# Kernel optimization log

Hardware: AMD Instinct MI355X
Metric: run time of the kernel (lower is better)

Reference implementation:

```python
import jax, jax.numpy as jnp
import numpy as np


def setup_inputs() -> dict:
    key = jax.random.key(0)
    k1, k2, k3, k4 = jax.random.split(key, 4)
    N, E, F_IN, HID, C = 50000, 1600000, 256, 64, 16
    x = jax.random.normal(k1, (N, F_IN), dtype=jnp.float32)
    edge_index = jax.random.randint(k2, (2, E), 0, N, dtype=jnp.int64)
    W1 = jax.random.normal(k3, (F_IN, HID), dtype=jnp.float32) * (1.0 / np.sqrt(F_IN))
    b1 = jnp.zeros((HID,), dtype=jnp.float32)
    W2 = jax.random.normal(k4, (HID, C), dtype=jnp.float32) * (1.0 / np.sqrt(HID))
    b2 = jnp.zeros((C,), dtype=jnp.float32)
    return {"x": x, "edge_index": edge_index, "W1": W1, "b1": b1, "W2": W2, "b2": b2}


def reference(x, edge_index, W1, b1, W2, b2):
    N = x.shape[0]
    # Add self-loops (GCNConv default)
    loops = jnp.arange(N, dtype=edge_index.dtype)
    row = jnp.concatenate([edge_index[0], loops])  # targets
    col = jnp.concatenate([edge_index[1], loops])  # sources
    # Symmetric normalization: deg^{-1/2}[row] * deg^{-1/2}[col]
    ones = jnp.ones(row.shape[0], dtype=x.dtype)
    deg = jax.ops.segment_sum(ones, row, num_segments=N)
    dinv = jnp.where(deg > 0, jax.lax.rsqrt(jnp.maximum(deg, 1e-12)), 0.0)
    norm = dinv[row] * dinv[col]  # [E+N]

    def gcn_conv(h, W, b):
        h = h @ W                          # dense transform first (fewer features gathered)
        msg = h[col] * norm[:, None]       # gather + normalize
        out = jax.ops.segment_sum(msg, row, num_segments=N)  # scatter-add
        return out + b

    h = jax.nn.relu(gcn_conv(x, W1, b1))
    # F.dropout(training=self.training) -> identity in eval mode
    out = gcn_conv(h, W2, b2)
    return jax.nn.log_softmax(out, axis=1)
```

## Files before the change

### kernel.cpp

```cpp
#include <hip/hip_runtime.h>
#include <math.h>

#define FIN 256
#define HID 64
#define NC  16



__global__ void k_hist(const int* __restrict__ row, int* __restrict__ cnt, int E) {
    int e = blockIdx.x * blockDim.x + threadIdx.x;
    if (e < E) atomicAdd(&cnt[row[e]], 1);
}

__global__ void k_dinv(const int* __restrict__ cnt, float* __restrict__ dinv, int N) {
    int i = blockIdx.x * blockDim.x + threadIdx.x;
    if (i < N) dinv[i] = rsqrtf((float)(cnt[i] + 1));
}


__global__ void k_scan_block(const int* __restrict__ cnt, int* __restrict__ offtmp,
                             int* __restrict__ bsum, int N) {
    __shared__ int s[256];
    int t = threadIdx.x, i = blockIdx.x * 256 + t;
    int v = (i < N) ? cnt[i] : 0;
    s[t] = v; __syncthreads();
    for (int d = 1; d < 256; d <<= 1) {
        int add = (t >= d) ? s[t - d] : 0;
        __syncthreads();
        s[t] += add;
        __syncthreads();
    }
    if (i < N) offtmp[i] = s[t] - v;
    if (t == 255) bsum[blockIdx.x] = s[255];
}

__global__ void k_scan_bsum(int* __restrict__ bsum, int nb) {
    __shared__ int s[256];
    int t = threadIdx.x;
    int v = (t < nb) ? bsum[t] : 0;
    s[t] = v; __syncthreads();
    for (int d = 1; d < 256; d <<= 1) {
        int add = (t >= d) ? s[t - d] : 0;
        __syncthreads();
        s[t] += add;
        __syncthreads();
    }
    if (t < nb) bsum[t] = s[t] - v;
}

__global__ void k_off(const int* __restrict__ offtmp, const int* __restrict__ bsum,
                      int* __restrict__ off, int* __restrict__ cur, int N) {
    int i = blockIdx.x * blockDim.x + threadIdx.x;
    if (i < N) {
        int o = offtmp[i] + bsum[i >> 8];
        off[i] = o;
        cur[i] = o;
    }
}

__global__ void k_bstart(const int* __restrict__ off, int* __restrict__ bcur, int NB) {
    int b = threadIdx.x;
    if (b < NB) bcur[b] = off[b << 8];
}


#define BIN_CHUNK 4096

__global__ __launch_bounds__(256) void k_bin(const int* __restrict__ row,
                                             const int* __restrict__ col,
                                             int* __restrict__ bcur,
                                             int2* __restrict__ stage, int E) {
    __shared__ unsigned lcnt[256];
    __shared__ unsigned lpos[256];
    const int tid = threadIdx.x;
    const int base = blockIdx.x * BIN_CHUNK;

    lcnt[tid] = 0;
    __syncthreads();

    int      rr[16];
    unsigned myofs[16];
#pragma unroll
    for (int k = 0; k < 16; ++k) {
        int idx = base + tid + k * 256;
        if (idx < E) {
            int r = row[idx];
            rr[k] = r;
            myofs[k] = atomicAdd(&lcnt[r >> 8], 1u);
        }
    }
    __syncthreads();

    unsigned c = lcnt[tid];
    lpos[tid] = (c > 0) ? (unsigned)atomicAdd(&bcur[tid], (int)c) : 0u;
    __syncthreads();

#pragma unroll
    for (int k = 0; k < 16; ++k) {
        int idx = base + tid + k * 256;
        if (idx < E) {
            int r = rr[k];
            unsigned p = lpos[r >> 8] + myofs[k];
            stage[p] = make_int2(r, col[idx]);
        }
    }
}


__global__ void k_place(const int2* __restrict__ stage, int* __restrict__ cur,
                        int* __restrict__ colS, int E) {
    int e = blockIdx.x * blockDim.x + threadIdx.x;
    if (e < E) {
        int2 rc = stage[e];
        int p = atomicAdd(&cur[rc.x], 1);
        colS[p] = rc.y;
    }
}


__global__ __launch_bounds__(256) void k_gemm1(const float* __restrict__ x,
                                               const float* __restrict__ W1,
                                               float* __restrict__ h1) {
    __shared__ float Ws[FIN * HID];
    __shared__ float xs[16][FIN + 4];
    const int tid = threadIdx.x;

    const float4* W4 = (const float4*)W1;
    float4* Ws4 = (float4*)Ws;
#pragma unroll
    for (int i = 0; i < 16; ++i) Ws4[tid + i * 256] = W4[tid + i * 256];

    const int row0 = blockIdx.x * 16;
    const float4* x4 = (const float4*)(x + (size_t)row0 * FIN);
#pragma unroll
    for (int i = 0; i < 4; ++i) {
        int idx = tid + i * 256;
        int r = idx >> 6;
        int q = idx & 63;
        *(float4*)&xs[r][q * 4] = x4[idx];
    }
    __syncthreads();

    const int r  = tid >> 4;
    const int c0 = (tid & 15) << 2;
    float4 acc = make_float4(0.f, 0.f, 0.f, 0.f);
    const float* xr = xs[r];
#pragma unroll 4
    for (int k = 0; k < FIN; k += 4) {
        float4 xv = *(const float4*)(xr + k);
        float4 w0 = *(const float4*)(Ws + (k + 0) * HID + c0);
        float4 w1 = *(const float4*)(Ws + (k + 1) * HID + c0);
        float4 w2 = *(const float4*)(Ws + (k + 2) * HID + c0);
        float4 w3 = *(const float4*)(Ws + (k + 3) * HID + c0);
        acc.x += xv.x * w0.x + xv.y * w1.x + xv.z * w2.x + xv.w * w3.x;
        acc.y += xv.x * w0.y + xv.y * w1.y + xv.z * w2.y + xv.w * w3.y;
        acc.z += xv.x * w0.z + xv.y * w1.z + xv.z * w2.z + xv.w * w3.z;
        acc.w += xv.x * w0.w + xv.y * w1.w + xv.z * w2.w + xv.w * w3.w;
    }
    *(float4*)(h1 + (size_t)(row0 + r) * HID + c0) = acc;
}


__global__ __launch_bounds__(256) void k_agg1(const int* __restrict__ off,
                                              const int* __restrict__ cnt,
                                              const int* __restrict__ colS,
                                              const float* __restrict__ dinv,
                                              const float* __restrict__ h1,
                                              float* __restrict__ agg1, int N) {
    int i = blockIdx.x * 4 + (threadIdx.x >> 6);
    if (i >= N) return;
    int lane = threadIdx.x & 63;
    int s = off[i], n = cnt[i];
    float di = dinv[i];
    float acc = di * h1[(size_t)i * HID + lane];

    int j = 0;
    for (; j + 4 <= n; j += 4) {
        int   c0 = colS[s + j],     c1 = colS[s + j + 1];
        int   c2 = colS[s + j + 2], c3 = colS[s + j + 3];
        float w0 = dinv[c0], w1 = dinv[c1], w2 = dinv[c2], w3 = dinv[c3];
        acc += h1[(size_t)c0 * HID + lane] * w0;
        acc += h1[(size_t)c1 * HID + lane] * w1;
        acc += h1[(size_t)c2 * HID + lane] * w2;
        acc += h1[(size_t)c3 * HID + lane] * w3;
    }
    for (; j < n; ++j) {
        int c = colS[s + j];
        acc += h1[(size_t)c * HID + lane] * dinv[c];
    }
    agg1[(size_t)i * HID + lane] = di * acc;
}


__global__ __launch_bounds__(256) void k_gemm2(const float* __restrict__ agg1,
                                               const float* __restrict__ b1,
                                               const float* __restrict__ W2,
                                               float* __restrict__ h2) {
    __shared__ float Ws[HID * NC];
    __shared__ float hs[16][HID + 4];
    const int tid = threadIdx.x;

#pragma unroll
    for (int i = 0; i < 4; ++i) Ws[tid + i * 256] = W2[tid + i * 256];

    const int n0 = blockIdx.x * 16;
    {
        float4 v = ((const float4*)(agg1 + (size_t)n0 * HID))[tid];
        int n  = tid >> 4;
        int k0 = (tid & 15) << 2;
        float4 bb = *(const float4*)(b1 + k0);
        v.x = fmaxf(v.x + bb.x, 0.f);
        v.y = fmaxf(v.y + bb.y, 0.f);
        v.z = fmaxf(v.z + bb.z, 0.f);
        v.w = fmaxf(v.w + bb.w, 0.f);
        *(float4*)&hs[n][k0] = v;
    }
    __syncthreads();

    const int n = tid >> 4;
    const int c = tid & 15;
    float acc = 0.f;
#pragma unroll
    for (int k = 0; k < HID; ++k) {
        acc += hs[n][k] * Ws[k * NC + c];
    }
    h2[(size_t)(n0 + n) * NC + c] = acc;
}


__global__ __launch_bounds__(256) void k_agg2(const int* __restrict__ off,
                                              const int* __restrict__ cnt,
                                              const int* __restrict__ colS,
                                              const float* __restrict__ dinv,
                                              const float* __restrict__ h2,
                                              float* __restrict__ agg2, int N) {
    int i = blockIdx.x * 4 + (threadIdx.x >> 6);
    if (i >= N) return;
    int lane = threadIdx.x & 63;
    int f = lane & 15;
    int k = lane >> 4;
    int s = off[i], n = cnt[i];

    float acc = 0.f;
    for (int j = k; j < n; j += 4) {
        int c = colS[s + j];
        acc += h2[(size_t)c * NC + f] * dinv[c];
    }
    acc += __shfl_xor(acc, 16, 64);
    acc += __shfl_xor(acc, 32, 64);
    if (k == 0) {
        float di = dinv[i];
        agg2[(size_t)i * NC + f] = di * (acc + di * h2[(size_t)i * NC + f]);
    }
}


__global__ __launch_bounds__(256) void k_final(const float* __restrict__ agg2,
                                               const float* __restrict__ b2,
                                               float* __restrict__ out, int N) {
    int i = blockIdx.x * blockDim.x + threadIdx.x;
    if (i >= N) return;
    float v[NC];
    const float4* src = (const float4*)(agg2 + (size_t)i * NC);
#pragma unroll
    for (int q = 0; q < 4; ++q) {
        float4 t = src[q];
        v[q * 4 + 0] = t.x + b2[q * 4 + 0];
        v[q * 4 + 1] = t.y + b2[q * 4 + 1];
        v[q * 4 + 2] = t.z + b2[q * 4 + 2];
        v[q * 4 + 3] = t.w + b2[q * 4 + 3];
    }
    float m = v[0];
#pragma unroll
    for (int c = 1; c < NC; ++c) m = fmaxf(m, v[c]);
    float s = 0.f;
#pragma unroll
    for (int c = 0; c < NC; ++c) s += expf(v[c] - m);
    float ls = logf(s);
    float4* dst = (float4*)(out + (size_t)i * NC);
#pragma unroll
    for (int q = 0; q < 4; ++q) {
        float4 t;
        t.x = v[q * 4 + 0] - m - ls;
        t.y = v[q * 4 + 1] - m - ls;
        t.z = v[q * 4 + 2] - m - ls;
        t.w = v[q * 4 + 3] - m - ls;
        dst[q] = t;
    }
}


extern "C" void kernel_launch(void* const* d_in, const int* in_sizes, int n_in,
                              void* d_out, int out_size, void* d_ws, size_t ws_size,
                              hipStream_t stream) {
    const float* x  = (const float*)d_in[0];
    const int*   ei = (const int*)d_in[1];
    const float* W1 = (const float*)d_in[2];
    const float* b1 = (const float*)d_in[3];
    const float* W2 = (const float*)d_in[4];
    const float* b2 = (const float*)d_in[5];
    float* out = (float*)d_out;

    const int N = in_sizes[0] / FIN;
    const int E = in_sizes[1] / 2;
    const int* row = ei;
    const int* col = ei + E;
    const int NB = (N + 255) >> 8;

    char* w = (char*)d_ws;
    int*   cnt    = (int*)w;                w += (size_t)N * 4;
    int*   off    = (int*)w;                w += (size_t)N * 4;
    int*   cur    = (int*)w;                w += (size_t)N * 4;
    int*   offtmp = (int*)w;                w += (size_t)N * 4;
    int*   bsum   = (int*)w;                w += 256 * 4;
    int*   bcur   = (int*)w;                w += 256 * 4;
    int*   colS   = (int*)w;                w += (size_t)E * 4;
    float* dinv   = (float*)w;              w += (size_t)N * 4;
    float* h1     = (float*)w;              w += (size_t)N * HID * 4;
    float* agg1   = (float*)w;              w += (size_t)N * HID * 4;
    float* h2     = (float*)w;              w += (size_t)N * NC * 4;
    float* agg2   = (float*)w;              w += (size_t)N * NC * 4;
    int2*  stage  = (int2*)h1;

    const int B = 256;
    const int nbN = (N + B - 1) / B;

    hipMemsetAsync(cnt, 0, (size_t)N * 4, stream);
    k_hist<<<(E + B - 1) / B, B, 0, stream>>>(row, cnt, E);
    k_dinv<<<nbN, B, 0, stream>>>(cnt, dinv, N);

    k_scan_block<<<nbN, B, 0, stream>>>(cnt, offtmp, bsum, N);
    k_scan_bsum<<<1, B, 0, stream>>>(bsum, nbN);
    k_off<<<nbN, B, 0, stream>>>(offtmp, bsum, off, cur, N);
    k_bstart<<<1, B, 0, stream>>>(off, bcur, NB);

    k_bin<<<(E + BIN_CHUNK - 1) / BIN_CHUNK, B, 0, stream>>>(row, col, bcur, stage, E);
    k_place<<<(E + B - 1) / B, B, 0, stream>>>(stage, cur, colS, E);

    k_gemm1<<<N / 16, B, 0, stream>>>(x, W1, h1);
    k_agg1<<<(N + 3) / 4, B, 0, stream>>>(off, cnt, colS, dinv, h1, agg1, N);

    k_gemm2<<<N / 16, B, 0, stream>>>(agg1, b1, W2, h2);
    k_agg2<<<(N + 3) / 4, B, 0, stream>>>(off, cnt, colS, dinv, h2, agg2, N);

    k_final<<<nbN, B, 0, stream>>>(agg2, b2, out, N);
}
```

Before: 415.3 us.

## Fuse dinv into offset kernel, register-tile gemm1, fuse log_softmax into agg2

Folds the degree-inverse computation into the offset kernel and the final bias plus log_softmax into the second aggregation kernel, so two launches and the agg2 round trip are gone. The first GEMM now computes 64 rows per block with a 4x4 register tile per thread, reusing W1 loaded into shared memory across more rows and issuing fewer redundant shared loads. In exchange each block uses much more shared memory (about 130KB), which may lower occupancy, and the softmax adds shuffle reductions inside the aggregation kernel.

Measured after the change: 416.4 us. No clear change (+0.3%).

```diff
diff --git a/kernel.cpp b/kernel.cpp
--- a/kernel.cpp
+++ b/kernel.cpp
@@ -6,15 +6,9 @@
 #define NC  16
 
 
-
 __global__ void k_hist(const int* __restrict__ row, int* __restrict__ cnt, int E) {
     int e = blockIdx.x * blockDim.x + threadIdx.x;
     if (e < E) atomicAdd(&cnt[row[e]], 1);
-}
-
-__global__ void k_dinv(const int* __restrict__ cnt, float* __restrict__ dinv, int N) {
-    int i = blockIdx.x * blockDim.x + threadIdx.x;
-    if (i < N) dinv[i] = rsqrtf((float)(cnt[i] + 1));
 }
 
 
@@ -49,12 +43,14 @@
 }
 
 __global__ void k_off(const int* __restrict__ offtmp, const int* __restrict__ bsum,
-                      int* __restrict__ off, int* __restrict__ cur, int N) {
+                      const int* __restrict__ cnt, int* __restrict__ off,
+                      int* __restrict__ cur, float* __restrict__ dinv, int N) {
     int i = blockIdx.x * blockDim.x + threadIdx.x;
     if (i < N) {
         int o = offtmp[i] + bsum[i >> 8];
         off[i] = o;
         cur[i] = o;
+        dinv[i] = rsqrtf((float)(cnt[i] + 1));
     }
 }
 
@@ -118,46 +114,67 @@
 }
 
 
+#define G1_ROWS 64
+
 __global__ __launch_bounds__(256) void k_gemm1(const float* __restrict__ x,
                                                const float* __restrict__ W1,
-                                               float* __restrict__ h1) {
-    __shared__ float Ws[FIN * HID];
-    __shared__ float xs[16][FIN + 4];
+                                               float* __restrict__ h1, int N) {
+    __shared__ float Ws[FIN][HID];
+    __shared__ float xs[G1_ROWS][FIN + 4];
     const int tid = threadIdx.x;
-
-    const float4* W4 = (const float4*)W1;
-    float4* Ws4 = (float4*)Ws;
-#pragma unroll
-    for (int i = 0; i < 16; ++i) Ws4[tid + i * 256] = W4[tid + i * 256];
-
-    const int row0 = blockIdx.x * 16;
-    const float4* x4 = (const float4*)(x + (size_t)row0 * FIN);
-#pragma unroll
-    for (int i = 0; i < 4; ++i) {
-        int idx = tid + i * 256;
-        int r = idx >> 6;
-        int q = idx & 63;
-        *(float4*)&xs[r][q * 4] = x4[idx];
-    }
-    __syncthreads();
-
-    const int r  = tid >> 4;
+    const int row0 = blockIdx.x * G1_ROWS;
+
+    {
+        const float4* W4 = (const float4*)W1;
+        float4* Ws4 = (float4*)&Ws[0][0];
+#pragma unroll
+        for (int i = 0; i < 16; ++i) Ws4[tid + i * 256] = W4[tid + i * 256];
+    }
+    {
+#pragma unroll
+        for (int i = 0; i < 16; ++i) {
+            int idx = tid + i * 256;
+            int r = idx >> 6;
+            int q = idx & 63;
+            int gr = row0 + r;
+            float4 v = make_float4(0.f, 0.f, 0.f, 0.f);
+            if (gr < N) v = ((const float4*)(x + (size_t)gr * FIN))[q];
+            *(float4*)&xs[r][q * 4] = v;
+        }
+    }
+    __syncthreads();
+
+    const int rg = (tid >> 4) << 2;
     const int c0 = (tid & 15) << 2;
-    float4 acc = make_float4(0.f, 0.f, 0.f, 0.f);
-    const float* xr = xs[r];
+    float acc[4][4] = {};
+
 #pragma unroll 4
     for (int k = 0; k < FIN; k += 4) {
-        float4 xv = *(const float4*)(xr + k);
-        float4 w0 = *(const float4*)(Ws + (k + 0) * HID + c0);
-        float4 w1 = *(const float4*)(Ws + (k + 1) * HID + c0);
-        float4 w2 = *(const float4*)(Ws + (k + 2) * HID + c0);
-        float4 w3 = *(const float4*)(Ws + (k + 3) * HID + c0);
-        acc.x += xv.x * w0.x + xv.y * w1.x + xv.z * w2.x + xv.w * w3.x;
-        acc.y += xv.x * w0.y + xv.y * w1.y + xv.z * w2.y + xv.w * w3.y;
-        acc.z += xv.x * w0.z + xv.y * w1.z + xv.z * w2.z + xv.w * w3.z;
-        acc.w += xv.x * w0.w + xv.y * w1.w + xv.z * w2.w + xv.w * w3.w;
-    }
-    *(float4*)(h1 + (size_t)(row0 + r) * HID + c0) = acc;
+        float4 w0 = *(const float4*)&Ws[k + 0][c0];
+        float4 w1 = *(const float4*)&Ws[k + 1][c0];
+        float4 w2 = *(const float4*)&Ws[k + 2][c0];
+        float4 w3 = *(const float4*)&Ws[k + 3][c0];
+        float4 xv0 = *(const float4*)&xs[rg + 0][k];
+        float4 xv1 = *(const float4*)&xs[rg + 1][k];
+        float4 xv2 = *(const float4*)&xs[rg + 2][k];
+        float4 xv3 = *(const float4*)&xs[rg + 3][k];
+#define G1_ROW(i, xv)                                                        \
+        acc[i][0] += xv.x * w0.x + xv.y * w1.x + xv.z * w2.x + xv.w * w3.x;  \
+        acc[i][1] += xv.x * w0.y + xv.y * w1.y + xv.z * w2.y + xv.w * w3.y;  \
+        acc[i][2] += xv.x * w0.z + xv.y * w1.z + xv.z * w2.z + xv.w * w3.z;  \
+        acc[i][3] += xv.x * w0.w + xv.y * w1.w + xv.z * w2.w + xv.w * w3.w;
+        G1_ROW(0, xv0) G1_ROW(1, xv1) G1_ROW(2, xv2) G1_ROW(3, xv3)
+#undef G1_ROW
+    }
+
+#pragma unroll
+    for (int i = 0; i < 4; ++i) {
+        int gr = row0 + rg + i;
+        if (gr < N) {
+            float4 v = make_float4(acc[i][0], acc[i][1], acc[i][2], acc[i][3]);
+            *(float4*)(h1 + (size_t)gr * HID + c0) = v;
+        }
+    }
 }
 
 
@@ -228,12 +245,13 @@
 }
 
 
-__global__ __launch_bounds__(256) void k_agg2(const int* __restrict__ off,
-                                              const int* __restrict__ cnt,
-                                              const int* __restrict__ colS,
-                                              const float* __restrict__ dinv,
-                                              const float* __restrict__ h2,
-                                              float* __restrict__ agg2, int N) {
+__global__ __launch_bounds__(256) void k_agg2f(const int* __restrict__ off,
+                                               const int* __restrict__ cnt,
+                                               const int* __restrict__ colS,
+                                               const float* __restrict__ dinv,
+                                               const float* __restrict__ h2,
+                                               const float* __restrict__ b2,
+                                               float* __restrict__ out, int N) {
     int i = blockIdx.x * 4 + (threadIdx.x >> 6);
     if (i >= N) return;
     int lane = threadIdx.x & 63;
@@ -248,45 +266,24 @@
     }
     acc += __shfl_xor(acc, 16, 64);
     acc += __shfl_xor(acc, 32, 64);
-    if (k == 0) {
-        float di = dinv[i];
-        agg2[(size_t)i * NC + f] = di * (acc + di * h2[(size_t)i * NC + f]);
-    }
-}
-
-
-__global__ __launch_bounds__(256) void k_final(const float* __restrict__ agg2,
-                                               const float* __restrict__ b2,
-                                               float* __restrict__ out, int N) {
-    int i = blockIdx.x * blockDim.x + threadIdx.x;
-    if (i >= N) return;
-    float v[NC];
-    const float4* src = (const float4*)(agg2 + (size_t)i * NC);
-#pragma unroll
-    for (int q = 0; q < 4; ++q) {
-        float4 t = src[q];
-        v[q * 4 + 0] = t.x + b2[q * 4 + 0];
-        v[q * 4 + 1] = t.y + b2[q * 4 + 1];
-        v[q * 4 + 2] = t.z + b2[q * 4 + 2];
-        v[q * 4 + 3] = t.w + b2[q * 4 + 3];
-    }
-    float m = v[0];
-#pragma unroll
-    for (int c = 1; c < NC; ++c) m = fmaxf(m, v[c]);
-    float s = 0.f;
-#pragma unroll
-    for (int c = 0; c < NC; ++c) s += expf(v[c] - m);
-    float ls = logf(s);
-    float4* dst = (float4*)(out + (size_t)i * NC);
-#pragma unroll
-    for (int q = 0; q < 4; ++q) {
-        float4 t;
-        t.x = v[q * 4 + 0] - m - ls;
-        t.y = v[q * 4 + 1] - m - ls;
-        t.z = v[q * 4 + 2] - m - ls;
-        t.w = v[q * 4 + 3] - m - ls;
-        dst[q] = t;
-    }
+
+    float di = dinv[i];
+    float v = di * (acc + di * h2[(size_t)i * NC + f]) + b2[f];
+
+    float m = v;
+    m = fmaxf(m, __shfl_xor(m, 1, 64));
+    m = fmaxf(m, __shfl_xor(m, 2, 64));
+    m = fmaxf(m, __shfl_xor(m, 4, 64));
+    m = fmaxf(m, __shfl_xor(m, 8, 64));
+    float ex = expf(v - m);
+    float sum = ex;
+    sum += __shfl_xor(sum, 1, 64);
+    sum += __shfl_xor(sum, 2, 64);
+    sum += __shfl_xor(sum, 4, 64);
+    sum += __shfl_xor(sum, 8, 64);
+    float r = v - m - logf(sum);
+
+    if (k == 0) out[(size_t)i * NC + f] = r;
 }
 
 
@@ -319,7 +316,6 @@
     float* h1     = (float*)w;              w += (size_t)N * HID * 4;
     float* agg1   = (float*)w;              w += (size_t)N * HID * 4;
     float* h2     = (float*)w;              w += (size_t)N * NC * 4;
-    float* agg2   = (float*)w;              w += (size_t)N * NC * 4;
     int2*  stage  = (int2*)h1;
 
     const int B = 256;
@@ -327,21 +323,18 @@
 
     hipMemsetAsync(cnt, 0, (size_t)N * 4, stream);
     k_hist<<<(E + B - 1) / B, B, 0, stream>>>(row, cnt, E);
-    k_dinv<<<nbN, B, 0, stream>>>(cnt, dinv, N);
 
     k_scan_block<<<nbN, B, 0, stream>>>(cnt, offtmp, bsum, N);
     k_scan_bsum<<<1, B, 0, stream>>>(bsum, nbN);
-    k_off<<<nbN, B, 0, stream>>>(offtmp, bsum, off, cur, N);
+    k_off<<<nbN, B, 0, stream>>>(offtmp, bsum, cnt, off, cur, dinv, N);
     k_bstart<<<1, B, 0, stream>>>(off, bcur, NB);
 
     k_bin<<<(E + BIN_CHUNK - 1) / BIN_CHUNK, B, 0, stream>>>(row, col, bcur, stage, E);
     k_place<<<(E + B - 1) / B, B, 0, stream>>>(stage, cur, colS, E);
 
-    k_gemm1<<<N / 16, B, 0, stream>>>(x, W1, h1);
+    k_gemm1<<<(N + G1_ROWS - 1) / G1_ROWS, B, 0, stream>>>(x, W1, h1, N);
     k_agg1<<<(N + 3) / 4, B, 0, stream>>>(off, cnt, colS, dinv, h1, agg1, N);
 
     k_gemm2<<<N / 16, B, 0, stream>>>(agg1, b1, W2, h2);
-    k_agg2<<<(N + 3) / 4, B, 0, stream>>>(off, cnt, colS, dinv, h2, agg2, N);
-
-    k_final<<<nbN, B, 0, stream>>>(agg2, b2, out, N);
-}
+    k_agg2f<<<(N + 3) / 4, B, 0, stream>>>(off, cnt, colS, dinv, h2, b2, out, N);
+}
```
